# Optimization experiments

Hardware: AMD Instinct MI355X
Metric: run time of the kernel (lower is better)

## Reference

```python
import jax, jax.numpy as jnp
import numpy as np

WS = (7, 7, 7)          # window size (S, H, W)
NUM_HEADS = 6
DIM = 192
B_, NW = 128, 32        # total windows, windows per image (mask dim)
N = WS[0] * WS[1] * WS[2]  # 343 tokens per window


def _relative_position_index():
    # Faithful replica of the torch __init__ logic (incl. indexing='xy' and
    # the 3*W1-1 / 2*W1-1 multipliers).
    cs = np.arange(WS[0]); ch = np.arange(WS[1]); cw = np.arange(WS[2])
    coords = np.stack(np.meshgrid(cs, ch, cw, indexing='xy'))  # (3, Wh, Ws, Ww)
    cf = coords.reshape(3, -1)                                  # (3, N)
    rel = cf[:, :, None] - cf[:, None, :]                       # (3, N, N)
    rel = rel.transpose(1, 2, 0).astype(np.int64)               # (N, N, 3)
    rel[:, :, 0] += WS[0] - 1
    rel[:, :, 1] += WS[1] - 1
    rel[:, :, 2] += WS[2] - 1
    rel[:, :, 0] *= 3 * WS[1] - 1
    rel[:, :, 1] *= 2 * WS[1] - 1
    return rel.sum(-1)                                          # (N, N) int


def setup_inputs() -> dict:
    key = jax.random.key(0)
    ks = jax.random.split(key, 6)
    C = DIM
    x = jax.random.normal(ks[0], (B_, N, C), dtype=jnp.float32)
    mask = jax.random.normal(ks[1], (NW, N, N), dtype=jnp.float32)
    qkv_w = jax.random.normal(ks[2], (3 * C, C), dtype=jnp.float32) * 0.02
    qkv_b = jnp.zeros((3 * C,), dtype=jnp.float32)
    proj_w = jax.random.normal(ks[3], (C, C), dtype=jnp.float32) * 0.02
    proj_b = jnp.zeros((C,), dtype=jnp.float32)
    table_len = (2 * WS[0] - 1) * (2 * WS[1] - 1) * (2 * WS[2] - 1)
    rpb_table = jax.random.normal(ks[4], (table_len, NUM_HEADS), dtype=jnp.float32) * 0.02
    rel_index = jnp.asarray(_relative_position_index(), dtype=jnp.int32)
    return {"x": x, "mask": mask, "qkv_w": qkv_w, "qkv_b": qkv_b,
            "proj_w": proj_w, "proj_b": proj_b, "rpb_table": rpb_table,
            "rel_index": rel_index}


def reference(x, mask, qkv_w, qkv_b, proj_w, proj_b, rpb_table, rel_index):
    B, n, C = x.shape
    H = NUM_HEADS
    hd = C // H
    scale = hd ** (-0.5)
    qkv = x @ qkv_w.T + qkv_b                      # (B, N, 3C)
    qkv = qkv.reshape(B, n, 3, H, hd).transpose(2, 0, 3, 1, 4)  # (3, B, H, N, hd)
    q, k, v = qkv[0] * scale, qkv[1], qkv[2]
    attn = jnp.einsum('bhnd,bhmd->bhnm', q, k)     # (B, H, N, N)
    bias = rpb_table[rel_index.reshape(-1)].reshape(n, n, H)
    attn = attn + bias.transpose(2, 0, 1)[None]    # (B, H, N, N)
    nW = mask.shape[0]
    attn = attn.reshape(B // nW, nW, H, n, n) + mask[None, :, None]
    attn = jax.nn.softmax(attn.reshape(B, H, n, n), axis=-1)
    out = jnp.einsum('bhnm,bhmd->bhnd', attn, v)   # (B, H, N, hd)
    out = out.transpose(0, 2, 1, 3).reshape(B, n, C)
    return out @ proj_w.T + proj_b
```

## Files before the change

### kernel.cpp

```cpp
#include <hip/hip_runtime.h>
#include <hip/hip_fp16.h>
#include <hip/hip_bf16.h>
#include <stdint.h>

#define WN 343
#define NH 6
#define HD 32
#define CD 192
#define NB 128
#define NWM 32
#define BMROW 352
#define BMSLICE (11*16*BMROW)
#define BMKC (16*BMROW)
#define LOG2E 1.4426950408889634f

typedef __attribute__((ext_vector_type(8))) short short8;
typedef __attribute__((ext_vector_type(4))) float f32x4;

__device__ __forceinline__ unsigned short f2bf(float f) {
  union { float f; uint32_t u; } v; v.f = f;
  uint32_t r = v.u + 0x7fffu + ((v.u >> 16) & 1u);
  return (unsigned short)(r >> 16);
}

__device__ __forceinline__ uint32_t pk2bf(float a, float b) {
  __hip_bfloat162 h = __float22bfloat162_rn(make_float2(a, b));
  return *(uint32_t*)&h;
}

__device__ __forceinline__ uint32_t pkh2(float a, float b) {
  __half2 h; h.x = __float2half(a); h.y = __float2half(b);
  return *(uint32_t*)&h;
}

typedef const __attribute__((address_space(1))) unsigned int* gas_ptr;
typedef __attribute__((address_space(3))) unsigned int* las_ptr;
__device__ __forceinline__ void gload16(const unsigned short* g, unsigned short* l) {
  __builtin_amdgcn_global_load_lds((gas_ptr)(const void*)g, (las_ptr)(void*)l, 16, 0, 0);
}

__global__ __launch_bounds__(256) void prep_kernel(
    const float* __restrict__ wq, const float* __restrict__ wp,
    unsigned short* __restrict__ wqb, unsigned short* __restrict__ wpb,
    const int* __restrict__ rel, const float* __restrict__ rpb,
    const float* __restrict__ mask, uint32_t* __restrict__ bP,
    uint32_t* __restrict__ mP, const float* __restrict__ x,
    unsigned short* __restrict__ xb) {
  __shared__ float M[352][33];
  const int bid = blockIdx.x;
  const int tid = threadIdx.x;
  if (bid < 66 + 352) {
    const bool isBias = (bid < 66);
    const int sub = isBias ? bid : bid - 66;
    const int grp = sub / 11;
    const int kc = sub - grp * 11;
    const int k0 = kc * 32;
    const float* mw = mask + (size_t)grp * (WN * WN);
    for (int idx = tid; idx < 352 * 32; idx += 256) {
      int n = idx >> 5, k = idx & 31;
      float v;
      if (isBias) {
        int nc = (n < WN) ? n : (WN - 1);
        v = (k0 + k < WN) ? rpb[rel[nc * WN + k0 + k] * NH + grp] * LOG2E
                          : -30000.0f;
      } else {
        v = (n < WN && k0 + k < WN) ? mw[n * WN + k0 + k] * LOG2E : 0.0f;
      }
      M[n][k] = v;
    }
    __syncthreads();
    uint32_t* outp = (isBias ? bP : mP) + (size_t)grp * BMSLICE + (size_t)kc * BMKC;
#pragma unroll
    for (int quad = 0; quad < 4; ++quad) {
#pragma unroll
      for (int j = 0; j < 2; ++j) {
        int n = tid + 256 * j;
        if (n < 352) {
          uint4 o;
          o.x = pkh2(M[n][quad * 8 + 0], M[n][quad * 8 + 4]);
          o.y = pkh2(M[n][quad * 8 + 1], M[n][quad * 8 + 5]);
          o.z = pkh2(M[n][quad * 8 + 2], M[n][quad * 8 + 6]);
          o.w = pkh2(M[n][quad * 8 + 3], M[n][quad * 8 + 7]);
          *(uint4*)(outp + ((size_t)quad * 352 + n) * 4) = o;
        }
      }
    }
    return;
  }
  int cb = bid - 418;
  if (cb < 54) {
    int g = cb * 256 + tid;
    int sk = g / 768; int rem = g - sk * 768;
    int row = rem >> 2; int cc = rem & 3;
    int s = sk / 6; int kt = sk - s * 6;
    int lch = cc ^ ((row >> 1) & 3);
    const float* src = wq + (size_t)(s * 192 + row) * CD + kt * 32 + lch * 8;
    f32x4 a = *(const f32x4*)src;
    f32x4 b = *(const f32x4*)(src + 4);
    union { short8 v8; uint32_t d[4]; } pk;
    pk.d[0] = pk2bf(a[0], a[1]);
    pk.d[1] = pk2bf(a[2], a[3]);
    pk.d[2] = pk2bf(b[0], b[1]);
    pk.d[3] = pk2bf(b[2], b[3]);
    *(short8*)(wqb + (size_t)g * 8) = pk.v8;
    return;
  }
  cb -= 54;
  if (cb < 18) {
    int g = cb * 256 + tid;
    int kt = g / 768; int rem = g - kt * 768;
    int row = rem >> 2; int cc = rem & 3;
    int lch = cc ^ ((row >> 1) & 3);
    const float* src = wp + (size_t)row * CD + kt * 32 + lch * 8;
    f32x4 a = *(const f32x4*)src;
    f32x4 b = *(const f32x4*)(src + 4);
    union { short8 v8; uint32_t d[4]; } pk;
    pk.d[0] = pk2bf(a[0], a[1]);
    pk.d[1] = pk2bf(a[2], a[3]);
    pk.d[2] = pk2bf(b[0], b[1]);
    pk.d[3] = pk2bf(b[2], b[3]);
    *(short8*)(wpb + (size_t)g * 8) = pk.v8;
    return;
  }
  cb -= 18;
  size_t gx = (size_t)cb * 256 + tid;
  int tile = (int)(gx >> 9); int rem = (int)(gx & 511);
  int row = rem >> 2; int cc = rem & 3;
  int mb = tile / 6; int kt = tile - mb * 6;
  int lch = cc ^ ((row >> 1) & 3);
  const float* src = x + ((size_t)mb * 128 + row) * CD + kt * 32 + lch * 8;
  f32x4 a = *(const f32x4*)src;
  f32x4 b = *(const f32x4*)(src + 4);
  union { short8 v8; uint32_t d[4]; } pk;
  pk.d[0] = pk2bf(a[0], a[1]);
  pk.d[1] = pk2bf(a[2], a[3]);
  pk.d[2] = pk2bf(b[0], b[1]);
  pk.d[3] = pk2bf(b[2], b[3]);
  *(short8*)(xb + gx * 8) = pk.v8;
}

__global__ __launch_bounds__(256) void bmfuse_kernel(
    const uint32_t* __restrict__ bP, const uint32_t* __restrict__ mP,
    uint32_t* __restrict__ bmP) {
  const int slice = blockIdx.y;
  const int wdx = slice / NH;
  const int h = slice - wdx * NH;
  int i = (blockIdx.x * 256 + threadIdx.x) * 4;
  if (i >= BMSLICE) return;
  uint4 bb = *(const uint4*)(bP + (size_t)h * BMSLICE + i);
  uint4 mm = *(const uint4*)(mP + (size_t)wdx * BMSLICE + i);
  uint4 o; __half2 t;
  t = __hadd2(*(__half2*)&bb.x, *(__half2*)&mm.x); o.x = *(uint32_t*)&t;
  t = __hadd2(*(__half2*)&bb.y, *(__half2*)&mm.y); o.y = *(uint32_t*)&t;
  t = __hadd2(*(__half2*)&bb.z, *(__half2*)&mm.z); o.z = *(uint32_t*)&t;
  t = __hadd2(*(__half2*)&bb.w, *(__half2*)&mm.w); o.w = *(uint32_t*)&t;
  *(uint4*)(bmP + (size_t)slice * BMSLICE + i) = o;
}

__global__ __launch_bounds__(256) void qkv_kernel(
    const unsigned short* __restrict__ xb, const unsigned short* __restrict__ wqb,
    const float* __restrict__ bvec,
    unsigned short* __restrict__ qb, unsigned short* __restrict__ kb,
    unsigned short* __restrict__ vb) {
  __shared__ __align__(16) unsigned short SL[10240];
  unsigned short* XL = SL;
  unsigned short* WL = SL + 4096;
  const int tid = threadIdx.x;
  const int wave = tid >> 6, lane = tid & 63;
  const int quad = lane >> 4, c = lane & 15;
  const int m0 = blockIdx.x * 128;
  const int s = blockIdx.y;
  const int chk = (quad ^ ((c >> 1) & 3)) * 8;

  f32x4 acc[2][12];
#pragma unroll
  for (int i = 0; i < 2; ++i)
#pragma unroll
    for (int j = 0; j < 12; ++j) acc[i][j] = (f32x4){0.f, 0.f, 0.f, 0.f};

  const size_t xt0 = (size_t)blockIdx.x * 6;
  const size_t wt0 = (size_t)s * 6;
  for (int kt = 0; kt < 6; ++kt) {
    const unsigned short* gx = xb + ((xt0 + kt) << 12) + tid * 8;
    const unsigned short* gw = wqb + (wt0 + kt) * 6144 + tid * 8;
    unsigned short* lx = XL + (size_t)wave * 512;
    unsigned short* lw = WL + (size_t)wave * 512;
    gload16(gx, lx);
    gload16(gx + 2048, lx + 2048);
    gload16(gw, lw);
    gload16(gw + 2048, lw + 2048);
    gload16(gw + 4096, lw + 4096);
    __syncthreads();
    short8 af0 = *(const short8*)&XL[(wave * 32 + c) * 32 + chk];
    short8 af1 = *(const short8*)&XL[(wave * 32 + 16 + c) * 32 + chk];
#pragma unroll
    for (int j = 0; j < 12; ++j) {
      short8 bfr = *(const short8*)&WL[(j * 16 + c) * 32 + chk];
      acc[0][j] = __builtin_amdgcn_mfma_f32_16x16x32_bf16(af0, bfr, acc[0][j], 0, 0, 0);
      acc[1][j] = __builtin_amdgcn_mfma_f32_16x16x32_bf16(af1, bfr, acc[1][j], 0, 0, 0);
    }
    __syncthreads();
  }

  const float qscale = 0.25503486f;
  unsigned short* dst = (s == 0) ? qb : ((s == 1) ? kb : vb);
  const float scl = (s == 0) ? qscale : 1.0f;
  const int n0 = s * 192;
  unsigned short* Lh0 = SL;
  unsigned short* Lh1 = SL + 4608;
  for (int hh = 0; hh < 3; ++hh) {
    __syncthreads();
#pragma unroll
    for (int jj = 0; jj < 4; ++jj) {
      int j = hh * 4 + jj;
      int hl = jj >> 1;
      int dd = (jj & 1) * 16 + c;
      float bn = bvec[n0 + j * 16 + c];
      unsigned short* L = hl ? Lh1 : Lh0;
#pragma unroll
      for (int i = 0; i < 2; ++i)
#pragma unroll
        for (int r = 0; r < 4; ++r) {
          int m = wave * 32 + i * 16 + quad * 4 + r;
          L[m * 36 + dd] = f2bf((acc[i][j][r] + bn) * scl);
        }
    }
    __syncthreads();
    const int m = tid & 127;
    const int hl = tid >> 7;
    const int M = m0 + m;
    const int b = M / WN;
    const int tok = M - b * WN;
    const int h = hh * 2 + hl;
    const unsigned short* L = hl ? Lh1 : Lh0;
    unsigned short* drow = dst + (((size_t)b * NH + h) * WN + tok) * HD;
#pragma unroll
    for (int t2 = 0; t2 < 4; ++t2) {
      int d0 = t2 * 8;
      *(short8*)&drow[d0] = *(const short8*)&L[m * 36 + d0];
    }
  }
}

__global__ __launch_bounds__(512) void attn_kernel(
    const unsigned short* __restrict__ qb, const unsigned short* __restrict__ kb,
    const unsigned short* __restrict__ vb, const uint32_t* __restrict__ bmP,
    unsigned short* __restrict__ ob) {
  __shared__ __align__(16) unsigned short Ks[352][40];
  __shared__ __align__(16) unsigned short Vt[HD][360];
  const int bid = blockIdx.x;
  const int job = (bid & 7) * 96 + (bid >> 3);
  const int wdx = job / 24;
  const int inner = job - wdx * 24;
  const int h = inner >> 2;
  const int b = (inner & 3) * 32 + wdx;
  const int tid = threadIdx.x;
  const int wave = tid >> 6, lane = tid & 63;
  const int quad = lane >> 4, c = lane & 15;
  const size_t base = ((size_t)b * NH + h) * (WN * HD);
  const unsigned short* q = qb + base;
  const unsigned short* k = kb + base;
  const unsigned short* v = vb + base;
  const uint32_t* bmS = bmP + (size_t)(wdx * 6 + h) * BMSLICE;

  for (int t = tid; t < WN * 4; t += 512) {
    int r = t >> 2, ch = t & 3;
    int kk = r & 31;
    int row = (r & ~31) + 16 * ((kk >> 2) & 1) + 4 * (kk >> 3) + (kk & 3);
    *(short8*)&Ks[row][ch * 8] = *(const short8*)(k + r * HD + ch * 8);
  }
  for (int t = tid; t < 9 * 32; t += 512) {
    int kg = WN + (t >> 5);
    int kk = kg & 31;
    int row = (kg & ~31) + 16 * ((kk >> 2) & 1) + 4 * (kk >> 3) + (kk & 3);
    Ks[row][t & 31] = 0;
  }
  for (int t = tid; t < WN; t += 512) {
#pragma unroll
    for (int ch = 0; ch < 4; ++ch) {
      short8 vv = *(const short8*)(v + t * HD + ch * 8);
#pragma unroll
      for (int j = 0; j < 8; ++j) Vt[ch * 8 + j][t] = vv[j];
    }
  }
  for (int t = tid; t < 9 * 32; t += 512) {
    Vt[t & 31][WN + (t >> 5)] = 0;
  }
  __syncthreads();

  for (int qt = wave; qt < 22; qt += 8) {
    const int q0 = qt * 16;
    int qr = q0 + c; if (qr > WN - 1) qr = WN - 1;
    const short8 qf = *(const short8*)(q + qr * HD + quad * 8);
    const uint32_t* bmRow = bmS + ((size_t)quad * 352 + q0 + c) * 4;

    f32x4 o0 = (f32x4){0.f, 0.f, 0.f, 0.f}, o1 = (f32x4){0.f, 0.f, 0.f, 0.f};
    float l = 0.f;
#pragma unroll
    for (int kc = 0; kc < 11; ++kc) {
      uint4 w4 = *(const uint4*)(bmRow + (size_t)kc * BMKC);
      f32x4 cc0, cc1;
      {
        float2 f;
        f = __half22float2(*(__half2*)&w4.x); cc0[0] = f.x; cc1[0] = f.y;
        f = __half22float2(*(__half2*)&w4.y); cc0[1] = f.x; cc1[1] = f.y;
        f = __half22float2(*(__half2*)&w4.z); cc0[2] = f.x; cc1[2] = f.y;
        f = __half22float2(*(__half2*)&w4.w); cc0[3] = f.x; cc1[3] = f.y;
      }
      const int k0 = kc * 32;
      short8 kf0 = *(const short8*)&Ks[k0 + c][quad * 8];
      short8 kf1 = *(const short8*)&Ks[k0 + 16 + c][quad * 8];
      f32x4 s0 = __builtin_amdgcn_mfma_f32_16x16x32_bf16(kf0, qf, cc0, 0, 0, 0);
      f32x4 s1 = __builtin_amdgcn_mfma_f32_16x16x32_bf16(kf1, qf, cc1, 0, 0, 0);
      float p0 = __builtin_amdgcn_exp2f(s0[0]), p1 = __builtin_amdgcn_exp2f(s0[1]);
      float p2 = __builtin_amdgcn_exp2f(s0[2]), p3 = __builtin_amdgcn_exp2f(s0[3]);
      float p4 = __builtin_amdgcn_exp2f(s1[0]), p5 = __builtin_amdgcn_exp2f(s1[1]);
      float p6 = __builtin_amdgcn_exp2f(s1[2]), p7 = __builtin_amdgcn_exp2f(s1[3]);
      l += (p0 + p1 + p2 + p3) + (p4 + p5 + p6 + p7);
      union { short8 v8; uint32_t d[4]; } pf;
      pf.d[0] = pk2bf(p0, p1);
      pf.d[1] = pk2bf(p2, p3);
      pf.d[2] = pk2bf(p4, p5);
      pf.d[3] = pk2bf(p6, p7);
      short8 vf0 = *(const short8*)&Vt[c][k0 + quad * 8];
      short8 vf1 = *(const short8*)&Vt[16 + c][k0 + quad * 8];
      o0 = __builtin_amdgcn_mfma_f32_16x16x32_bf16(pf.v8, vf0, o0, 0, 0, 0);
      o1 = __builtin_amdgcn_mfma_f32_16x16x32_bf16(pf.v8, vf1, o1, 0, 0, 0);
    }
    l += __shfl_xor(l, 16);
    l += __shfl_xor(l, 32);

#pragma unroll
    for (int r = 0; r < 4; ++r) {
      int n = q0 + quad * 4 + r;
      if (n < WN) {
        float lq = __shfl(l, quad * 4 + r, 16);
        float inv = 1.0f / lq;
        int M = b * WN + n;
        int rloc = M & 127;
        int xr = (rloc >> 1) & 3;
        size_t base2 = (((size_t)(M >> 7) * 6 + h) << 12) + rloc * 32;
        ob[base2 + (((c >> 3) ^ xr) << 3) + (c & 7)] = f2bf(o0[r] * inv);
        ob[base2 + ((((c >> 3) | 2) ^ xr) << 3) + (c & 7)] = f2bf(o1[r] * inv);
      }
    }
  }
}

__global__ __launch_bounds__(256) void proj_kernel(
    const unsigned short* __restrict__ obp, const unsigned short* __restrict__ wpb,
    const float* __restrict__ bvec, float* __restrict__ out) {
  __shared__ __align__(16) unsigned short SL[8192];
  unsigned short* XL = SL;
  unsigned short* WL = SL + 2048;
  const int tid = threadIdx.x;
  const int wave = tid >> 6, lane = tid & 63;
  const int quad = lane >> 4, c = lane & 15;
  const int m0 = blockIdx.x * 64;
  const int mb = blockIdx.x >> 1;
  const int r0 = (blockIdx.x & 1) * 64;
  const int chk = (quad ^ ((c >> 1) & 3)) * 8;

  f32x4 acc[12];
#pragma unroll
  for (int j = 0; j < 12; ++j) acc[j] = (f32x4){0.f, 0.f, 0.f, 0.f};

  for (int kt = 0; kt < 6; ++kt) {
    const unsigned short* gx =
        obp + (((size_t)mb * 6 + kt) << 12) + r0 * 32 + tid * 8;
    const unsigned short* gw = wpb + (size_t)kt * 6144 + tid * 8;
    unsigned short* lx = XL + (size_t)wave * 512;
    unsigned short* lw = WL + (size_t)wave * 512;
    gload16(gx, lx);
    gload16(gw, lw);
    gload16(gw + 2048, lw + 2048);
    gload16(gw + 4096, lw + 4096);
    __syncthreads();
    short8 af = *(const short8*)&XL[(wave * 16 + c) * 32 + chk];
#pragma unroll
    for (int j = 0; j < 12; ++j) {
      short8 bfr = *(const short8*)&WL[(j * 16 + c) * 32 + chk];
      acc[j] = __builtin_amdgcn_mfma_f32_16x16x32_bf16(af, bfr, acc[j], 0, 0, 0);
    }
    __syncthreads();
  }

#pragma unroll
  for (int j = 0; j < 12; ++j) {
    int col = j * 16 + c;
    float bn = bvec[col];
#pragma unroll
    for (int r = 0; r < 4; ++r) {
      int m = m0 + wave * 16 + quad * 4 + r;
      out[(size_t)m * CD + col] = acc[j][r] + bn;
    }
  }
}

extern "C" void kernel_launch(void* const* d_in, const int* in_sizes, int n_in,
                              void* d_out, int out_size, void* d_ws, size_t ws_size,
                              hipStream_t stream) {
  const float* x      = (const float*)d_in[0];
  const float* mask   = (const float*)d_in[1];
  const float* qkv_w  = (const float*)d_in[2];
  const float* qkv_b  = (const float*)d_in[3];
  const float* proj_w = (const float*)d_in[4];
  const float* proj_b = (const float*)d_in[5];
  const float* rpb    = (const float*)d_in[6];
  const int*   rel    = (const int*)d_in[7];
  float* out = (float*)d_out;

  char* ws = (char*)d_ws;
  uint32_t* biasP = (uint32_t*)ws;
  size_t off = 1486848;
  uint32_t* maskP = (uint32_t*)(ws + off); off += 7929856;
  uint32_t* bmP   = (uint32_t*)(ws + off); off += 47579136;
  unsigned short* qb = (unsigned short*)(ws + off); off += 16859136;
  unsigned short* kb = (unsigned short*)(ws + off); off += 16859136;
  unsigned short* vb = (unsigned short*)(ws + off); off += 16859136;
  unsigned short* wqb = (unsigned short*)(ws + off); off += 221184;
  unsigned short* wpb = (unsigned short*)(ws + off); off += 73728;
  unsigned short* xb  = (unsigned short*)(ws + off); off += 16859136;
  unsigned short* obuf = xb;

  hipLaunchKernelGGL(prep_kernel, dim3(418 + 54 + 18 + 4116), dim3(256), 0, stream,
                     qkv_w, proj_w, wqb, wpb, rel, rpb, mask, biasP, maskP, x, xb);
  hipLaunchKernelGGL(bmfuse_kernel, dim3(61, 192), dim3(256), 0, stream,
                     biasP, maskP, bmP);
  hipLaunchKernelGGL(qkv_kernel, dim3(343, 3), dim3(256), 0, stream,
                     xb, wqb, qkv_b, qb, kb, vb);
  hipLaunchKernelGGL(attn_kernel, dim3(NH * NB), dim3(512), 0, stream,
                     qb, kb, vb, bmP, obuf);
  hipLaunchKernelGGL(proj_kernel, dim3(686), dim3(256), 0, stream,
                     obuf, wpb, proj_b, out);
}
```

Measured before the change: 234.8 us.

## Fuse bias+mask add into attention kernel and drop materialized bias-mask buffer

Removes the separate bmfuse kernel that wrote a 47MB combined bias+mask fp16 tensor. The attention kernel now loads the per-head bias and per-window mask tiles separately and adds them with half2 ops in registers. The prep kernel is split into a conversion kernel and a bias/mask packing kernel, with the bias packing spread over more blocks. The kc loop unroll drops to 2, and attention issues twice as many global loads, though these come from smaller, more cache-friendly arrays.

```diff
diff --git a/kernel.cpp b/kernel.cpp
--- a/kernel.cpp
+++ b/kernel.cpp
@@ -39,55 +39,78 @@
   __builtin_amdgcn_global_load_lds((gas_ptr)(const void*)g, (las_ptr)(void*)l, 16, 0, 0);
 }
 
-__global__ __launch_bounds__(256) void prep_kernel(
-    const float* __restrict__ wq, const float* __restrict__ wp,
-    unsigned short* __restrict__ wqb, unsigned short* __restrict__ wpb,
+__global__ __launch_bounds__(256) void prep_bm_kernel(
     const int* __restrict__ rel, const float* __restrict__ rpb,
     const float* __restrict__ mask, uint32_t* __restrict__ bP,
-    uint32_t* __restrict__ mP, const float* __restrict__ x,
-    unsigned short* __restrict__ xb) {
+    uint32_t* __restrict__ mP) {
   __shared__ float M[352][33];
   const int bid = blockIdx.x;
   const int tid = threadIdx.x;
-  if (bid < 66 + 352) {
-    const bool isBias = (bid < 66);
-    const int sub = isBias ? bid : bid - 66;
-    const int grp = sub / 11;
-    const int kc = sub - grp * 11;
+  if (bid < 264) {
+    const int h = bid / 44;
+    const int rem = bid - h * 44;
+    const int kc = rem >> 2;
+    const int g = rem & 3;
+    const int n0 = g * 88;
     const int k0 = kc * 32;
-    const float* mw = mask + (size_t)grp * (WN * WN);
-    for (int idx = tid; idx < 352 * 32; idx += 256) {
-      int n = idx >> 5, k = idx & 31;
-      float v;
-      if (isBias) {
-        int nc = (n < WN) ? n : (WN - 1);
-        v = (k0 + k < WN) ? rpb[rel[nc * WN + k0 + k] * NH + grp] * LOG2E
-                          : -30000.0f;
-      } else {
-        v = (n < WN && k0 + k < WN) ? mw[n * WN + k0 + k] * LOG2E : 0.0f;
+    for (int idx = tid; idx < 88 * 32; idx += 256) {
+      int nl = idx >> 5, k = idx & 31;
+      int n = n0 + nl;
+      int nc = (n < WN) ? n : (WN - 1);
+      M[nl][k] = (k0 + k < WN) ? rpb[rel[nc * WN + k0 + k] * NH + h] * LOG2E
+                               : -30000.0f;
+    }
+    __syncthreads();
+    uint32_t* outp = bP + (size_t)h * BMSLICE + (size_t)kc * BMKC;
+    if (tid < 88) {
+      const int nl = tid;
+      const int n = n0 + nl;
+#pragma unroll
+      for (int quad = 0; quad < 4; ++quad) {
+        uint4 o;
+        o.x = pkh2(M[nl][quad * 8 + 0], M[nl][quad * 8 + 4]);
+        o.y = pkh2(M[nl][quad * 8 + 1], M[nl][quad * 8 + 5]);
+        o.z = pkh2(M[nl][quad * 8 + 2], M[nl][quad * 8 + 6]);
+        o.w = pkh2(M[nl][quad * 8 + 3], M[nl][quad * 8 + 7]);
+        *(uint4*)(outp + ((size_t)quad * 352 + n) * 4) = o;
       }
-      M[n][k] = v;
-    }
-    __syncthreads();
-    uint32_t* outp = (isBias ? bP : mP) + (size_t)grp * BMSLICE + (size_t)kc * BMKC;
-#pragma unroll
-    for (int quad = 0; quad < 4; ++quad) {
-#pragma unroll
-      for (int j = 0; j < 2; ++j) {
-        int n = tid + 256 * j;
-        if (n < 352) {
-          uint4 o;
-          o.x = pkh2(M[n][quad * 8 + 0], M[n][quad * 8 + 4]);
-          o.y = pkh2(M[n][quad * 8 + 1], M[n][quad * 8 + 5]);
-          o.z = pkh2(M[n][quad * 8 + 2], M[n][quad * 8 + 6]);
-          o.w = pkh2(M[n][quad * 8 + 3], M[n][quad * 8 + 7]);
-          *(uint4*)(outp + ((size_t)quad * 352 + n) * 4) = o;
-        }
+    }
+    return;
+  }
+  const int sub = bid - 264;
+  const int wdx = sub / 11;
+  const int kc = sub - wdx * 11;
+  const int k0 = kc * 32;
+  const float* mw = mask + (size_t)wdx * (WN * WN);
+  for (int idx = tid; idx < 352 * 32; idx += 256) {
+    int n = idx >> 5, k = idx & 31;
+    M[n][k] = (n < WN && k0 + k < WN) ? mw[n * WN + k0 + k] * LOG2E : 0.0f;
+  }
+  __syncthreads();
+  uint32_t* outp = mP + (size_t)wdx * BMSLICE + (size_t)kc * BMKC;
+#pragma unroll
+  for (int quad = 0; quad < 4; ++quad) {
+#pragma unroll
+    for (int j = 0; j < 2; ++j) {
+      int n = tid + 256 * j;
+      if (n < 352) {
+        uint4 o;
+        o.x = pkh2(M[n][quad * 8 + 0], M[n][quad * 8 + 4]);
+        o.y = pkh2(M[n][quad * 8 + 1], M[n][quad * 8 + 5]);
+        o.z = pkh2(M[n][quad * 8 + 2], M[n][quad * 8 + 6]);
+        o.w = pkh2(M[n][quad * 8 + 3], M[n][quad * 8 + 7]);
+        *(uint4*)(outp + ((size_t)quad * 352 + n) * 4) = o;
       }
     }
-    return;
-  }
-  int cb = bid - 418;
+  }
+}
+
+__global__ __launch_bounds__(256) void prep_cvt_kernel(
+    const float* __restrict__ wq, const float* __restrict__ wp,
+    const float* __restrict__ x, unsigned short* __restrict__ wqb,
+    unsigned short* __restrict__ wpb, unsigned short* __restrict__ xb) {
+  const int tid = threadIdx.x;
+  int cb = blockIdx.x;
   if (cb < 54) {
     int g = cb * 256 + tid;
     int sk = g / 768; int rem = g - sk * 768;
@@ -139,24 +162,6 @@
   *(short8*)(xb + gx * 8) = pk.v8;
 }
 
-__global__ __launch_bounds__(256) void bmfuse_kernel(
-    const uint32_t* __restrict__ bP, const uint32_t* __restrict__ mP,
-    uint32_t* __restrict__ bmP) {
-  const int slice = blockIdx.y;
-  const int wdx = slice / NH;
-  const int h = slice - wdx * NH;
-  int i = (blockIdx.x * 256 + threadIdx.x) * 4;
-  if (i >= BMSLICE) return;
-  uint4 bb = *(const uint4*)(bP + (size_t)h * BMSLICE + i);
-  uint4 mm = *(const uint4*)(mP + (size_t)wdx * BMSLICE + i);
-  uint4 o; __half2 t;
-  t = __hadd2(*(__half2*)&bb.x, *(__half2*)&mm.x); o.x = *(uint32_t*)&t;
-  t = __hadd2(*(__half2*)&bb.y, *(__half2*)&mm.y); o.y = *(uint32_t*)&t;
-  t = __hadd2(*(__half2*)&bb.z, *(__half2*)&mm.z); o.z = *(uint32_t*)&t;
-  t = __hadd2(*(__half2*)&bb.w, *(__half2*)&mm.w); o.w = *(uint32_t*)&t;
-  *(uint4*)(bmP + (size_t)slice * BMSLICE + i) = o;
-}
-
 __global__ __launch_bounds__(256) void qkv_kernel(
     const unsigned short* __restrict__ xb, const unsigned short* __restrict__ wqb,
     const float* __restrict__ bvec,
@@ -244,8 +249,8 @@
 
 __global__ __launch_bounds__(512) void attn_kernel(
     const unsigned short* __restrict__ qb, const unsigned short* __restrict__ kb,
-    const unsigned short* __restrict__ vb, const uint32_t* __restrict__ bmP,
-    unsigned short* __restrict__ ob) {
+    const unsigned short* __restrict__ vb, const uint32_t* __restrict__ biasP,
+    const uint32_t* __restrict__ maskP, unsigned short* __restrict__ ob) {
   __shared__ __align__(16) unsigned short Ks[352][40];
   __shared__ __align__(16) unsigned short Vt[HD][360];
   const int bid = blockIdx.x;
@@ -261,7 +266,8 @@
   const unsigned short* q = qb + base;
   const unsigned short* k = kb + base;
   const unsigned short* v = vb + base;
-  const uint32_t* bmS = bmP + (size_t)(wdx * 6 + h) * BMSLICE;
+  const uint32_t* bS = biasP + (size_t)h * BMSLICE;
+  const uint32_t* mS = maskP + (size_t)wdx * BMSLICE;
 
   for (int t = tid; t < WN * 4; t += 512) {
     int r = t >> 2, ch = t & 3;
@@ -292,20 +298,26 @@
     const int q0 = qt * 16;
     int qr = q0 + c; if (qr > WN - 1) qr = WN - 1;
     const short8 qf = *(const short8*)(q + qr * HD + quad * 8);
-    const uint32_t* bmRow = bmS + ((size_t)quad * 352 + q0 + c) * 4;
+    const uint32_t* bRow = bS + ((size_t)quad * 352 + q0 + c) * 4;
+    const uint32_t* mRow = mS + ((size_t)quad * 352 + q0 + c) * 4;
 
     f32x4 o0 = (f32x4){0.f, 0.f, 0.f, 0.f}, o1 = (f32x4){0.f, 0.f, 0.f, 0.f};
     float l = 0.f;
-#pragma unroll
+#pragma unroll 2
     for (int kc = 0; kc < 11; ++kc) {
-      uint4 w4 = *(const uint4*)(bmRow + (size_t)kc * BMKC);
+      uint4 bw4 = *(const uint4*)(bRow + (size_t)kc * BMKC);
+      uint4 mw4 = *(const uint4*)(mRow + (size_t)kc * BMKC);
       f32x4 cc0, cc1;
       {
-        float2 f;
-        f = __half22float2(*(__half2*)&w4.x); cc0[0] = f.x; cc1[0] = f.y;
-        f = __half22float2(*(__half2*)&w4.y); cc0[1] = f.x; cc1[1] = f.y;
-        f = __half22float2(*(__half2*)&w4.z); cc0[2] = f.x; cc1[2] = f.y;
-        f = __half22float2(*(__half2*)&w4.w); cc0[3] = f.x; cc1[3] = f.y;
+        __half2 s2; float2 f;
+        s2 = __hadd2(*(__half2*)&bw4.x, *(__half2*)&mw4.x);
+        f = __half22float2(s2); cc0[0] = f.x; cc1[0] = f.y;
+        s2 = __hadd2(*(__half2*)&bw4.y, *(__half2*)&mw4.y);
+        f = __half22float2(s2); cc0[1] = f.x; cc1[1] = f.y;
+        s2 = __hadd2(*(__half2*)&bw4.z, *(__half2*)&mw4.z);
+        f = __half22float2(s2); cc0[2] = f.x; cc1[2] = f.y;
+        s2 = __hadd2(*(__half2*)&bw4.w, *(__half2*)&mw4.w);
+        f = __half22float2(s2); cc0[3] = f.x; cc1[3] = f.y;
       }
       const int k0 = kc * 32;
       short8 kf0 = *(const short8*)&Ks[k0 + c][quad * 8];
@@ -414,7 +426,6 @@
   uint32_t* biasP = (uint32_t*)ws;
   size_t off = 1486848;
   uint32_t* maskP = (uint32_t*)(ws + off); off += 7929856;
-  uint32_t* bmP   = (uint32_t*)(ws + off); off += 47579136;
   unsigned short* qb = (unsigned short*)(ws + off); off += 16859136;
   unsigned short* kb = (unsigned short*)(ws + off); off += 16859136;
   unsigned short* vb = (unsigned short*)(ws + off); off += 16859136;
@@ -423,14 +434,14 @@
   unsigned short* xb  = (unsigned short*)(ws + off); off += 16859136;
   unsigned short* obuf = xb;
 
-  hipLaunchKernelGGL(prep_kernel, dim3(418 + 54 + 18 + 4116), dim3(256), 0, stream,
-                     qkv_w, proj_w, wqb, wpb, rel, rpb, mask, biasP, maskP, x, xb);
-  hipLaunchKernelGGL(bmfuse_kernel, dim3(61, 192), dim3(256), 0, stream,
-                     biasP, maskP, bmP);
+  hipLaunchKernelGGL(prep_cvt_kernel, dim3(54 + 18 + 4116), dim3(256), 0, stream,
+                     qkv_w, proj_w, x, wqb, wpb, xb);
+  hipLaunchKernelGGL(prep_bm_kernel, dim3(264 + 352), dim3(256), 0, stream,
+                     rel, rpb, mask, biasP, maskP);
   hipLaunchKernelGGL(qkv_kernel, dim3(343, 3), dim3(256), 0, stream,
                      xb, wqb, qkv_b, qb, kb, vb);
   hipLaunchKernelGGL(attn_kernel, dim3(NH * NB), dim3(512), 0, stream,
-                     qb, kb, vb, bmP, obuf);
+                     qb, kb, vb, biasP, maskP, obuf);
   hipLaunchKernelGGL(proj_kernel, dim3(686), dim3(256), 0, stream,
                      obuf, wpb, proj_b, out);
 }
```

New measurement: 219.6 us. -6.5%, faster.
